# Optimization experiments

Hardware: AMD Instinct MI355X
Metric: run time of the kernel (lower is better)

## Reference

```python
import jax, jax.numpy as jnp
import numpy as np

B, G, D, H, KD, E = 64, 512, 128, 8, 16, 128
NS = 20  # num_station


def _init_w(key, shape):
    stdv = 1.0 / np.sqrt(shape[-1]).astype(np.float32)
    return jax.random.uniform(key, shape, jnp.float32, -stdv, stdv)


def setup_inputs() -> dict:
    key = jax.random.key(0)
    ks = jax.random.split(key, 12)
    return {
        "q": jax.random.normal(ks[0], (B, G, D), jnp.float32),
        "h": jax.random.normal(ks[1], (B, G, D), jnp.float32),
        "W_query_depot": _init_w(ks[2], (H, D, KD)),
        "W_key_custom": _init_w(ks[3], (H, D, KD)),
        "W_val_custom": _init_w(ks[4], (H, D, KD)),
        "W_query_station": _init_w(ks[5], (H, D, KD)),
        "W_key_other": _init_w(ks[6], (H, D, KD)),
        "W_val_other": _init_w(ks[7], (H, D, KD)),
        "W_query_custom": _init_w(ks[8], (H, D, KD)),
        "W_key_all": _init_w(ks[9], (H, D, KD)),
        "W_val_all": _init_w(ks[10], (H, D, KD)),
        "W_out": _init_w(ks[11], (H, KD, E)),
        "num_station": NS,
    }


def _mha_block(q_seg, h_seg, Wq, Wk, Wv, norm):
    # q_seg: [B, Nq, D], h_seg: [B, Nk, D]; weights: [H, D, KD]
    Q = jnp.einsum('bqd,hdk->hbqk', q_seg, Wq)
    K = jnp.einsum('bnd,hdk->hbnk', h_seg, Wk)
    V = jnp.einsum('bnd,hdk->hbnk', h_seg, Wv)
    attn = jax.nn.softmax(norm * jnp.einsum('hbqk,hbnk->hbqn', Q, K), axis=-1)
    return jnp.einsum('hbqn,hbnk->hbqk', attn, V)  # [H, B, Nq, KD]


def reference(q, h, W_query_depot, W_key_custom, W_val_custom,
              W_query_station, W_key_other, W_val_other,
              W_query_custom, W_key_all, W_val_all, W_out, num_station):
    ns = num_station
    norm = 1.0 / np.sqrt(W_query_depot.shape[-1]).astype(np.float32)
    h_custom = h[:, 1 + ns:]                                        # customers
    h_other = jnp.concatenate([h[:, :1], h[:, 1 + ns:]], axis=1)    # depot + customers
    heads_depot = _mha_block(q[:, :1], h_custom,
                             W_query_depot, W_key_custom, W_val_custom, norm)
    heads_station = _mha_block(q[:, 1:1 + ns], h_other,
                               W_query_station, W_key_other, W_val_other, norm)
    heads_custom = _mha_block(q[:, 1 + ns:], h,
                              W_query_custom, W_key_all, W_val_all, norm)
    heads = jnp.concatenate([heads_depot, heads_station, heads_custom], axis=2)
    # final projection: mm([B*G, H*KD], [H*KD, E])
    return jnp.einsum('hbgk,hke->bge', heads, W_out)
```

## Files before the change

kernel.cpp:

```cpp
#include <hip/hip_runtime.h>
#include <hip/hip_bf16.h>

namespace {

typedef _Float16 v4h __attribute__((ext_vector_type(4)));
typedef __fp16   h2  __attribute__((ext_vector_type(2)));
typedef float    v4f __attribute__((ext_vector_type(4)));

constexpr int B = 64, G = 512, D = 128, H = 8, KD = 16, NS = 20;
constexpr float NORM = 0.25f;
constexpr float L2E  = 1.44269504088896f;
constexpr float MFIX = 16.0f;
constexpr int KP = 20;
constexpr int VP = 520;
constexpr int QCH = 256;

__device__ __forceinline__ v4f mfma16(v4h a, v4h b, v4f c) {
  return __builtin_amdgcn_mfma_f32_16x16x16f16(a, b, c, 0, 0, 0);
}
__device__ __forceinline__ v4h cvt4(float4 v) {
  h2 a = __builtin_amdgcn_cvt_pkrtz(v.x, v.y);
  h2 b = __builtin_amdgcn_cvt_pkrtz(v.z, v.w);
  return v4h{(_Float16)a[0], (_Float16)a[1], (_Float16)b[0], (_Float16)b[1]};
}
__device__ __forceinline__ v4h cvtacc(v4f v) {
  h2 a = __builtin_amdgcn_cvt_pkrtz(v[0], v[1]);
  h2 b = __builtin_amdgcn_cvt_pkrtz(v[2], v[3]);
  return v4h{(_Float16)a[0], (_Float16)a[1], (_Float16)b[0], (_Float16)b[1]};
}
__device__ __forceinline__ void pexp(v4f s0, v4f s1, v4h& p0, v4h& p1) {
  h2 e01 = __builtin_amdgcn_cvt_pkrtz(__builtin_amdgcn_exp2f(s0[0]),
                                      __builtin_amdgcn_exp2f(s0[1]));
  h2 e23 = __builtin_amdgcn_cvt_pkrtz(__builtin_amdgcn_exp2f(s0[2]),
                                      __builtin_amdgcn_exp2f(s0[3]));
  h2 e45 = __builtin_amdgcn_cvt_pkrtz(__builtin_amdgcn_exp2f(s1[0]),
                                      __builtin_amdgcn_exp2f(s1[1]));
  h2 e67 = __builtin_amdgcn_cvt_pkrtz(__builtin_amdgcn_exp2f(s1[2]),
                                      __builtin_amdgcn_exp2f(s1[3]));
  p0 = {(_Float16)e01[0], (_Float16)e01[1], (_Float16)e23[0], (_Float16)e23[1]};
  p1 = {(_Float16)e45[0], (_Float16)e45[1], (_Float16)e67[0], (_Float16)e67[1]};
}

struct SM {
  char      ht[8192];
  _Float16  Kl[512 * KP];
  _Float16  Vt[16 * VP];
};

template<int SEG, bool PAIR>
__device__ __forceinline__ void attn_loop(const SM& sm, int g, int c,
                                          v4h qfA, v4h qfB,
                                          v4f& oA, v4f& laA, v4f& oB, v4f& laB)
{
  constexpr int Ln  = SEG == 0 ? G - 1 - NS : SEG == 1 ? G - NS : G;
  constexpr int NCH = (Ln + 31) / 32;
  const _Float16* Kb = sm.Kl + c * KP + 4 * g;
  const _Float16* Vb = sm.Vt + c * VP + 4 * g;
  const v4f mc = {-MFIX, -MFIX, -MFIX, -MFIX};
  const v4h ones = {(_Float16)1.f, (_Float16)1.f, (_Float16)1.f, (_Float16)1.f};

  v4h k0 = *(const v4h*)(Kb);
  v4h k1 = *(const v4h*)(Kb + 16 * KP);
  v4f s0A = mfma16(k0, qfA, mc), s1A = mfma16(k1, qfA, mc);
  v4f s0B, s1B;
  if constexpr (PAIR) { s0B = mfma16(k0, qfB, mc); s1B = mfma16(k1, qfB, mc); }

  #pragma unroll
  for (int ch = 0; ch < NCH; ++ch) {
    const int nb = ch * 32;
    const v4h v0 = *(const v4h*)(Vb + nb);
    const v4h v1 = *(const v4h*)(Vb + nb + 16);
    v4f n0A, n1A, n0B, n1B;
    if (ch + 1 < NCH) {
      k0 = *(const v4h*)(Kb + (nb + 32) * KP);
      k1 = *(const v4h*)(Kb + (nb + 48) * KP);
      n0A = mfma16(k0, qfA, mc); n1A = mfma16(k1, qfA, mc);
      if constexpr (PAIR) { n0B = mfma16(k0, qfB, mc); n1B = mfma16(k1, qfB, mc); }
    }
    if constexpr ((Ln & 31) != 0) {
      if (ch == NCH - 1) {
        #pragma unroll
        for (int r = 0; r < 4; ++r) {
          if (nb + 4 * g + r >= Ln)      { s0A[r] = -1e30f; if constexpr (PAIR) s0B[r] = -1e30f; }
          if (nb + 16 + 4 * g + r >= Ln) { s1A[r] = -1e30f; if constexpr (PAIR) s1B[r] = -1e30f; }
        }
      }
    }
    v4h p0, p1;
    pexp(s0A, s1A, p0, p1);
    oA  = mfma16(v0, p0, oA);
    oA  = mfma16(v1, p1, oA);
    laA = mfma16(ones, p0, laA);
    laA = mfma16(ones, p1, laA);
    if constexpr (PAIR) {
      pexp(s0B, s1B, p0, p1);
      oB  = mfma16(v0, p0, oB);
      oB  = mfma16(v1, p1, oB);
      laB = mfma16(ones, p0, laB);
      laB = mfma16(ones, p1, laB);
      s0B = n0B; s1B = n1B;
    }
    s0A = n0A; s1A = n1A;
  }
}

template<int SEG>
__device__ __forceinline__ void seg_body(
    int bid, const float* __restrict__ q, const float* __restrict__ hb,
    const float* __restrict__ Wq, const float* __restrict__ Wk,
    const float* __restrict__ Wv, float* __restrict__ heads, SM& sm)
{
  constexpr int Lq   = SEG == 0 ? 1 : SEG == 1 ? NS : G - 1 - NS;
  constexpr int QOFF = SEG == 0 ? 0 : SEG == 1 ? 1  : 1 + NS;
  constexpr int Ln   = SEG == 0 ? G - 1 - NS : SEG == 1 ? G - NS : G;
  constexpr int NQC  = (Lq + QCH - 1) / QCH;

  const int hh   = bid >> 6;
  const int b    = bid & 63;
  const int tid  = threadIdx.x;
  const int w    = tid >> 6;
  const int lane = tid & 63;
  const int g    = lane >> 4, c = lane & 15;

  float4 rg[2];

  {
    v4h wA[8];
    const float* Wt = (w < 4) ? Wk : Wv;
    #pragma unroll
    for (int dc = 0; dc < 8; ++dc)
      #pragma unroll
      for (int bb = 0; bb < 4; ++bb)
        wA[dc][bb] = (_Float16)Wt[((size_t)hh * D + dc * 16 + 4 * g + bb) * KD + c];

    const int wk = w & 3;
    #pragma unroll
    for (int i = 0; i < 2; ++i) {
      int idx = tid + i * 512, r = idx >> 5, jj = idx & 31;
      int nn = r < Ln ? r : Ln - 1;
      int hr;
      if (SEG == 0)      hr = nn + 1 + NS;
      else if (SEG == 1) hr = (nn == 0) ? 0 : nn + NS;
      else               hr = nn;
      rg[i] = ((const float4*)(hb + ((size_t)b * G + hr) * D))[jj];
    }
    for (int t = 0; t < 16; ++t) {
      __syncthreads();
      #pragma unroll
      for (int i = 0; i < 2; ++i) {
        int idx = tid + i * 512, r = idx >> 5, jj = idx & 31;
        *(v4h*)(sm.ht + r * 256 + ((8 * jj) ^ ((r & 7) << 4))) = cvt4(rg[i]);
      }
      if (t < 15) {
        #pragma unroll
        for (int i = 0; i < 2; ++i) {
          int idx = tid + i * 512, r = idx >> 5, jj = idx & 31;
          int n = (t + 1) * 32 + r;
          int nn = n < Ln ? n : Ln - 1;
          int hr;
          if (SEG == 0)      hr = nn + 1 + NS;
          else if (SEG == 1) hr = (nn == 0) ? 0 : nn + NS;
          else               hr = nn;
          rg[i] = ((const float4*)(hb + ((size_t)b * G + hr) * D))[jj];
        }
      }
      __syncthreads();
      const int sl = (wk - 2 * t) & 3;
      if (sl < 2) {
        const int tile = 2 * t + sl;
        v4f acc = {0.f, 0.f, 0.f, 0.f};
        #pragma unroll
        for (int dc = 0; dc < 8; ++dc) {
          const v4h a = *(const v4h*)(sm.ht + (sl * 16 + c) * 256 +
                                      ((32 * dc + 8 * g) ^ ((c & 7) << 4)));
          acc = mfma16(a, wA[dc], acc);
        }
        if (w < 4) {
          #pragma unroll
          for (int r = 0; r < 4; ++r)
            sm.Kl[(tile * 16 + 4 * g + r) * KP + c] = (_Float16)acc[r];
        } else {
          v4h vv = {(_Float16)acc[0], (_Float16)acc[1], (_Float16)acc[2], (_Float16)acc[3]};
          *(v4h*)(sm.Vt + c * VP + tile * 16 + 4 * g) = vv;
        }
      }
    }
  }

  for (int qc = 0; qc < NQC; ++qc) {
    const int qbase = qc * QCH;
    const int qcnt  = (Lq - qbase < QCH) ? (Lq - qbase) : QCH;
    const int nqt   = (qcnt + 15) >> 4;
    const int nri   = (qcnt + 31) >> 5;

    v4h wQ[8];
    #pragma unroll
    for (int dc = 0; dc < 8; ++dc)
      #pragma unroll
      for (int bb = 0; bb < 4; ++bb)
        wQ[dc][bb] = (_Float16)(Wq[((size_t)hh * D + dc * 16 + 4 * g + bb) * KD + c]
                                * (NORM * L2E));

    v4f accA = {0.f,0.f,0.f,0.f}, accB = {0.f,0.f,0.f,0.f};
    #pragma unroll
    for (int i = 0; i < 2; ++i) {
      int idx = tid + i * 512, r = idx >> 5, jj = idx & 31;
      int qs = qbase + r;
      int gq = QOFF + (qs < Lq ? qs : Lq - 1);
      rg[i] = ((const float4*)(q + ((size_t)b * G + gq) * D))[jj];
    }
    for (int ri = 0; ri < nri; ++ri) {
      __syncthreads();
      #pragma unroll
      for (int i = 0; i < 2; ++i) {
        int idx = tid + i * 512, r = idx >> 5, jj = idx & 31;
        *(v4h*)(sm.ht + r * 256 + ((8 * jj) ^ ((r & 7) << 4))) = cvt4(rg[i]);
      }
      if (ri + 1 < nri) {
        #pragma unroll
        for (int i = 0; i < 2; ++i) {
          int idx = tid + i * 512, r = idx >> 5, jj = idx & 31;
          int qs = qbase + (ri + 1) * 32 + r;
          int gq = QOFF + (qs < Lq ? qs : Lq - 1);
          rg[i] = ((const float4*)(q + ((size_t)b * G + gq) * D))[jj];
        }
      }
      __syncthreads();
      const int sl = (w - 2 * ri) & 7;
      if (sl < 2) {
        const int t = 2 * ri + sl;
        if (t < nqt) {
          v4f acc = {0.f, 0.f, 0.f, 0.f};
          #pragma unroll
          for (int dc = 0; dc < 8; ++dc) {
            const v4h a = *(const v4h*)(sm.ht + (sl * 16 + c) * 256 +
                                        ((32 * dc + 8 * g) ^ ((c & 7) << 4)));
            acc = mfma16(wQ[dc], a, acc);
          }
          if (t < 8) accA = acc; else accB = acc;
        }
      }
    }

    const int t0 = w, tB = w + 8;
    const bool hasA = t0 < nqt, hasB = tB < nqt;
    if (hasA) {
      v4h qfA = cvtacc(accA);
      v4h qfB = {};
      if (hasB) qfB = cvtacc(accB);
      v4f oA = {0.f,0.f,0.f,0.f}, laA = {0.f,0.f,0.f,0.f};
      v4f oB = {0.f,0.f,0.f,0.f}, laB = {0.f,0.f,0.f,0.f};
      if (hasB) attn_loop<SEG, true >(sm, g, c, qfA, qfB, oA, laA, oB, laB);
      else      attn_loop<SEG, false>(sm, g, c, qfA, qfA, oA, laA, oB, laB);
      {
        const float invA = 1.0f / laA[0];
        const int qloc = qbase + t0 * 16 + c;
        if (qloc < Lq) {
          float4 val = {oA[0]*invA, oA[1]*invA, oA[2]*invA, oA[3]*invA};
          *(float4*)(heads + ((size_t)b * G + QOFF + qloc) * 128 + hh * 16 + 4 * g) = val;
        }
      }
      if (hasB) {
        const float invB = 1.0f / laB[0];
        const int qloc = qbase + tB * 16 + c;
        if (qloc < Lq) {
          float4 val = {oB[0]*invB, oB[1]*invB, oB[2]*invB, oB[3]*invB};
          *(float4*)(heads + ((size_t)b * G + QOFF + qloc) * 128 + hh * 16 + 4 * g) = val;
        }
      }
    }
  }
}

__global__ __launch_bounds__(512, 4)
void fused_attn(const float* __restrict__ q, const float* __restrict__ hb,
                const float* __restrict__ Wqd, const float* __restrict__ Wkc,
                const float* __restrict__ Wvc, const float* __restrict__ Wqs,
                const float* __restrict__ Wko, const float* __restrict__ Wvo,
                const float* __restrict__ Wqc, const float* __restrict__ Wka,
                const float* __restrict__ Wva, float* __restrict__ heads)
{
  __shared__ SM sm;
  const int bid = blockIdx.x;
  if (bid < 512)       seg_body<2>(bid,        q, hb, Wqc, Wka, Wva, heads, sm);
  else if (bid < 1024) seg_body<1>(bid - 512,  q, hb, Wqs, Wko, Wvo, heads, sm);
  else                 seg_body<0>(bid - 1024, q, hb, Wqd, Wkc, Wvc, heads, sm);
}

__global__ __launch_bounds__(256)
void out_proj_kernel(float* __restrict__ data, const float* __restrict__ Wout)
{
  __shared__ _Float16 WlT[128 * 132];
  __shared__ _Float16 Ah [64 * 132];
  const int tid  = threadIdx.x;
  const int lane = tid & 63, w = tid >> 6;
  const int g = lane >> 4, c = lane & 15;
  const size_t rowbase = (size_t)blockIdx.x * 64;

  #pragma unroll
  for (int i = 0; i < 16; ++i) {
    int idx = tid + i * 256;
    int k = idx >> 5, c4 = (idx & 31) * 4;
    float4 v = ((const float4*)Wout)[idx];
    WlT[(c4 + 0) * 132 + k] = (_Float16)v.x;
    WlT[(c4 + 1) * 132 + k] = (_Float16)v.y;
    WlT[(c4 + 2) * 132 + k] = (_Float16)v.z;
    WlT[(c4 + 3) * 132 + k] = (_Float16)v.w;
  }
  #pragma unroll
  for (int i = 0; i < 8; ++i) {
    int idx = tid + i * 256;
    int r = idx >> 5, c4 = (idx & 31) * 4;
    float4 v = ((const float4*)(data + rowbase * 128))[idx];
    *(v4h*)(Ah + r * 132 + c4) = cvt4(v);
  }
  __syncthreads();

  v4h af[8];
  #pragma unroll
  for (int dc = 0; dc < 8; ++dc)
    af[dc] = *(const v4h*)(Ah + (w * 16 + c) * 132 + dc * 16 + 4 * g);
  #pragma unroll
  for (int ct = 0; ct < 8; ++ct) {
    v4f acc = {0.f, 0.f, 0.f, 0.f};
    #pragma unroll
    for (int dc = 0; dc < 8; ++dc) {
      const v4h bf = *(const v4h*)(WlT + (ct * 16 + c) * 132 + dc * 16 + 4 * g);
      acc = mfma16(af[dc], bf, acc);
    }
    #pragma unroll
    for (int r = 0; r < 4; ++r)
      data[(rowbase + w * 16 + 4 * g + r) * 128 + ct * 16 + c] = acc[r];
  }
}

}

extern "C" void kernel_launch(void* const* d_in, const int* in_sizes, int n_in,
                              void* d_out, int out_size, void* d_ws, size_t ws_size,
                              hipStream_t stream) {
  const float* q    = (const float*)d_in[0];
  const float* h    = (const float*)d_in[1];
  const float* Wqd  = (const float*)d_in[2];
  const float* Wkc  = (const float*)d_in[3];
  const float* Wvc  = (const float*)d_in[4];
  const float* Wqs  = (const float*)d_in[5];
  const float* Wko  = (const float*)d_in[6];
  const float* Wvo  = (const float*)d_in[7];
  const float* Wqc  = (const float*)d_in[8];
  const float* Wka  = (const float*)d_in[9];
  const float* Wva  = (const float*)d_in[10];
  const float* Wout = (const float*)d_in[11];
  float* out = (float*)d_out;

  fused_attn<<<3 * B * H, 512, 0, stream>>>(q, h, Wqd, Wkc, Wvc,
                                            Wqs, Wko, Wvo, Wqc, Wka, Wva, out);
  out_proj_kernel<<<G * B / 64, 256, 0, stream>>>(out, Wout);
}
```

Before: 68.46 us.

## Process all query tiles per wave in one pass over K/V

Removes the query-chunk loop so each wave projects and holds up to four query tiles in registers, then streams K and V from shared memory once for all of them. This cuts repeated LDS reads of K/V and an extra round of Q-projection barriers for the large segment. It raises register pressure (four output and sum accumulators live at once) and drops the prefetch of next-chunk score MFMAs, which may reduce latency hiding or cause spills.

```diff
diff --git a/kernel.cpp b/kernel.cpp
--- a/kernel.cpp
+++ b/kernel.cpp
@@ -13,7 +13,6 @@
 constexpr float MFIX = 16.0f;
 constexpr int KP = 20;
 constexpr int VP = 520;
-constexpr int QCH = 256;
 
 __device__ __forceinline__ v4f mfma16(v4h a, v4h b, v4f c) {
   return __builtin_amdgcn_mfma_f32_16x16x16f16(a, b, c, 0, 0, 0);
@@ -47,63 +46,6 @@
   _Float16  Vt[16 * VP];
 };
 
-template<int SEG, bool PAIR>
-__device__ __forceinline__ void attn_loop(const SM& sm, int g, int c,
-                                          v4h qfA, v4h qfB,
-                                          v4f& oA, v4f& laA, v4f& oB, v4f& laB)
-{
-  constexpr int Ln  = SEG == 0 ? G - 1 - NS : SEG == 1 ? G - NS : G;
-  constexpr int NCH = (Ln + 31) / 32;
-  const _Float16* Kb = sm.Kl + c * KP + 4 * g;
-  const _Float16* Vb = sm.Vt + c * VP + 4 * g;
-  const v4f mc = {-MFIX, -MFIX, -MFIX, -MFIX};
-  const v4h ones = {(_Float16)1.f, (_Float16)1.f, (_Float16)1.f, (_Float16)1.f};
-
-  v4h k0 = *(const v4h*)(Kb);
-  v4h k1 = *(const v4h*)(Kb + 16 * KP);
-  v4f s0A = mfma16(k0, qfA, mc), s1A = mfma16(k1, qfA, mc);
-  v4f s0B, s1B;
-  if constexpr (PAIR) { s0B = mfma16(k0, qfB, mc); s1B = mfma16(k1, qfB, mc); }
-
-  #pragma unroll
-  for (int ch = 0; ch < NCH; ++ch) {
-    const int nb = ch * 32;
-    const v4h v0 = *(const v4h*)(Vb + nb);
-    const v4h v1 = *(const v4h*)(Vb + nb + 16);
-    v4f n0A, n1A, n0B, n1B;
-    if (ch + 1 < NCH) {
-      k0 = *(const v4h*)(Kb + (nb + 32) * KP);
-      k1 = *(const v4h*)(Kb + (nb + 48) * KP);
-      n0A = mfma16(k0, qfA, mc); n1A = mfma16(k1, qfA, mc);
-      if constexpr (PAIR) { n0B = mfma16(k0, qfB, mc); n1B = mfma16(k1, qfB, mc); }
-    }
-    if constexpr ((Ln & 31) != 0) {
-      if (ch == NCH - 1) {
-        #pragma unroll
-        for (int r = 0; r < 4; ++r) {
-          if (nb + 4 * g + r >= Ln)      { s0A[r] = -1e30f; if constexpr (PAIR) s0B[r] = -1e30f; }
-          if (nb + 16 + 4 * g + r >= Ln) { s1A[r] = -1e30f; if constexpr (PAIR) s1B[r] = -1e30f; }
-        }
-      }
-    }
-    v4h p0, p1;
-    pexp(s0A, s1A, p0, p1);
-    oA  = mfma16(v0, p0, oA);
-    oA  = mfma16(v1, p1, oA);
-    laA = mfma16(ones, p0, laA);
-    laA = mfma16(ones, p1, laA);
-    if constexpr (PAIR) {
-      pexp(s0B, s1B, p0, p1);
-      oB  = mfma16(v0, p0, oB);
-      oB  = mfma16(v1, p1, oB);
-      laB = mfma16(ones, p0, laB);
-      laB = mfma16(ones, p1, laB);
-      s0B = n0B; s1B = n1B;
-    }
-    s0A = n0A; s1A = n1A;
-  }
-}
-
 template<int SEG>
 __device__ __forceinline__ void seg_body(
     int bid, const float* __restrict__ q, const float* __restrict__ hb,
@@ -113,7 +55,10 @@
   constexpr int Lq   = SEG == 0 ? 1 : SEG == 1 ? NS : G - 1 - NS;
   constexpr int QOFF = SEG == 0 ? 0 : SEG == 1 ? 1  : 1 + NS;
   constexpr int Ln   = SEG == 0 ? G - 1 - NS : SEG == 1 ? G - NS : G;
-  constexpr int NQC  = (Lq + QCH - 1) / QCH;
+  constexpr int NCH  = (Ln + 31) / 32;
+  constexpr int NQT  = (Lq + 15) / 16;
+  constexpr int NRI  = (Lq + 31) / 32;
+  constexpr int NRB  = (NRI + 3) / 4;
 
   const int hh   = bid >> 6;
   const int b    = bid & 63;
@@ -187,12 +132,8 @@
     }
   }
 
-  for (int qc = 0; qc < NQC; ++qc) {
-    const int qbase = qc * QCH;
-    const int qcnt  = (Lq - qbase < QCH) ? (Lq - qbase) : QCH;
-    const int nqt   = (qcnt + 15) >> 4;
-    const int nri   = (qcnt + 31) >> 5;
-
+  v4h qf[4] = {};
+  {
     v4h wQ[8];
     #pragma unroll
     for (int dc = 0; dc < 8; ++dc)
@@ -200,71 +141,98 @@
       for (int bb = 0; bb < 4; ++bb)
         wQ[dc][bb] = (_Float16)(Wq[((size_t)hh * D + dc * 16 + 4 * g + bb) * KD + c]
                                 * (NORM * L2E));
-
-    v4f accA = {0.f,0.f,0.f,0.f}, accB = {0.f,0.f,0.f,0.f};
     #pragma unroll
     for (int i = 0; i < 2; ++i) {
       int idx = tid + i * 512, r = idx >> 5, jj = idx & 31;
-      int qs = qbase + r;
-      int gq = QOFF + (qs < Lq ? qs : Lq - 1);
-      rg[i] = ((const float4*)(q + ((size_t)b * G + gq) * D))[jj];
-    }
-    for (int ri = 0; ri < nri; ++ri) {
-      __syncthreads();
-      #pragma unroll
-      for (int i = 0; i < 2; ++i) {
-        int idx = tid + i * 512, r = idx >> 5, jj = idx & 31;
-        *(v4h*)(sm.ht + r * 256 + ((8 * jj) ^ ((r & 7) << 4))) = cvt4(rg[i]);
-      }
-      if (ri + 1 < nri) {
-        #pragma unroll
-        for (int i = 0; i < 2; ++i) {
-          int idx = tid + i * 512, r = idx >> 5, jj = idx & 31;
-          int qs = qbase + (ri + 1) * 32 + r;
-          int gq = QOFF + (qs < Lq ? qs : Lq - 1);
-          rg[i] = ((const float4*)(q + ((size_t)b * G + gq) * D))[jj];
-        }
-      }
-      __syncthreads();
-      const int sl = (w - 2 * ri) & 7;
-      if (sl < 2) {
-        const int t = 2 * ri + sl;
-        if (t < nqt) {
-          v4f acc = {0.f, 0.f, 0.f, 0.f};
+      int qs = r < Lq ? r : Lq - 1;
+      rg[i] = ((const float4*)(q + ((size_t)b * G + QOFF + qs) * D))[jj];
+    }
+    #pragma unroll
+    for (int rb = 0; rb < NRB; ++rb) {
+      #pragma unroll
+      for (int rr = 0; rr < 4; ++rr) {
+        constexpr int UNUSED = 0; (void)UNUSED;
+        const int ri = rb * 4 + rr;
+        if (ri < NRI) {
+          __syncthreads();
           #pragma unroll
-          for (int dc = 0; dc < 8; ++dc) {
-            const v4h a = *(const v4h*)(sm.ht + (sl * 16 + c) * 256 +
-                                        ((32 * dc + 8 * g) ^ ((c & 7) << 4)));
-            acc = mfma16(wQ[dc], a, acc);
+          for (int i = 0; i < 2; ++i) {
+            int idx = tid + i * 512, r = idx >> 5, jj = idx & 31;
+            *(v4h*)(sm.ht + r * 256 + ((8 * jj) ^ ((r & 7) << 4))) = cvt4(rg[i]);
           }
-          if (t < 8) accA = acc; else accB = acc;
-        }
-      }
-    }
-
-    const int t0 = w, tB = w + 8;
-    const bool hasA = t0 < nqt, hasB = tB < nqt;
-    if (hasA) {
-      v4h qfA = cvtacc(accA);
-      v4h qfB = {};
-      if (hasB) qfB = cvtacc(accB);
-      v4f oA = {0.f,0.f,0.f,0.f}, laA = {0.f,0.f,0.f,0.f};
-      v4f oB = {0.f,0.f,0.f,0.f}, laB = {0.f,0.f,0.f,0.f};
-      if (hasB) attn_loop<SEG, true >(sm, g, c, qfA, qfB, oA, laA, oB, laB);
-      else      attn_loop<SEG, false>(sm, g, c, qfA, qfA, oA, laA, oB, laB);
-      {
-        const float invA = 1.0f / laA[0];
-        const int qloc = qbase + t0 * 16 + c;
+          if (ri + 1 < NRI) {
+            #pragma unroll
+            for (int i = 0; i < 2; ++i) {
+              int idx = tid + i * 512, r = idx >> 5, jj = idx & 31;
+              int qs = (ri + 1) * 32 + r;
+              if (qs >= Lq) qs = Lq - 1;
+              rg[i] = ((const float4*)(q + ((size_t)b * G + QOFF + qs) * D))[jj];
+            }
+          }
+          __syncthreads();
+          const int sl = (w - 2 * ri) & 7;
+          if (sl < 2) {
+            const int t = 2 * ri + sl;
+            if (t < NQT) {
+              v4f acc = {0.f, 0.f, 0.f, 0.f};
+              #pragma unroll
+              for (int dc = 0; dc < 8; ++dc) {
+                const v4h a = *(const v4h*)(sm.ht + (sl * 16 + c) * 256 +
+                                            ((32 * dc + 8 * g) ^ ((c & 7) << 4)));
+                acc = mfma16(wQ[dc], a, acc);
+              }
+              qf[rb] = cvtacc(acc);
+            }
+          }
+        }
+      }
+    }
+  }
+
+  {
+    const _Float16* Kb = sm.Kl + c * KP + 4 * g;
+    const _Float16* Vb = sm.Vt + c * VP + 4 * g;
+    const v4f mc = {-MFIX, -MFIX, -MFIX, -MFIX};
+    const v4h ones = {(_Float16)1.f, (_Float16)1.f, (_Float16)1.f, (_Float16)1.f};
+    v4f o[4]  = {{0.f,0.f,0.f,0.f},{0.f,0.f,0.f,0.f},{0.f,0.f,0.f,0.f},{0.f,0.f,0.f,0.f}};
+    v4f la[4] = {{0.f,0.f,0.f,0.f},{0.f,0.f,0.f,0.f},{0.f,0.f,0.f,0.f},{0.f,0.f,0.f,0.f}};
+    #pragma unroll
+    for (int ch = 0; ch < NCH; ++ch) {
+      const int nb = ch * 32;
+      const v4h k0 = *(const v4h*)(Kb + nb * KP);
+      const v4h k1 = *(const v4h*)(Kb + (nb + 16) * KP);
+      const v4h v0 = *(const v4h*)(Vb + nb);
+      const v4h v1 = *(const v4h*)(Vb + nb + 16);
+      #pragma unroll
+      for (int j = 0; j < 4; ++j) {
+        if (w + 8 * j < NQT) {
+          v4f s0 = mfma16(k0, qf[j], mc);
+          v4f s1 = mfma16(k1, qf[j], mc);
+          if constexpr ((Ln & 31) != 0) {
+            if (ch == NCH - 1) {
+              #pragma unroll
+              for (int r = 0; r < 4; ++r) {
+                if (nb + 4 * g + r >= Ln)      s0[r] = -1e30f;
+                if (nb + 16 + 4 * g + r >= Ln) s1[r] = -1e30f;
+              }
+            }
+          }
+          v4h p0, p1;
+          pexp(s0, s1, p0, p1);
+          o[j]  = mfma16(v0, p0, o[j]);
+          o[j]  = mfma16(v1, p1, o[j]);
+          la[j] = mfma16(ones, p0, la[j]);
+          la[j] = mfma16(ones, p1, la[j]);
+        }
+      }
+    }
+    #pragma unroll
+    for (int j = 0; j < 4; ++j) {
+      if (w + 8 * j < NQT) {
+        const float inv = 1.0f / la[j][0];
+        const int qloc = (w + 8 * j) * 16 + c;
         if (qloc < Lq) {
-          float4 val = {oA[0]*invA, oA[1]*invA, oA[2]*invA, oA[3]*invA};
-          *(float4*)(heads + ((size_t)b * G + QOFF + qloc) * 128 + hh * 16 + 4 * g) = val;
-        }
-      }
-      if (hasB) {
-        const float invB = 1.0f / laB[0];
-        const int qloc = qbase + tB * 16 + c;
-        if (qloc < Lq) {
-          float4 val = {oB[0]*invB, oB[1]*invB, oB[2]*invB, oB[3]*invB};
+          float4 val = {o[j][0]*inv, o[j][1]*inv, o[j][2]*inv, o[j][3]*inv};
           *(float4*)(heads + ((size_t)b * G + QOFF + qloc) * 128 + hh * 16 + 4 * g) = val;
         }
       }
```

Measured after the change: 70.36 us. +2.8%, slower.

## Split Q/K/V projections into a separate kernel writing fp16 workspace

Applied to the files above, without the earlier changes.

Projections are moved out of the per-(segment, head, batch) attention blocks into a dedicated proj_kernel. Each block of that kernel loads a 64-row slice of h and q once and computes K/V for all three segments and all heads, plus Q, writing fp16 results to the workspace. The attention kernel then only loads precomputed K/V/Q from the workspace into LDS. This removes the repeated reading and projecting of h by every head and segment block. The cost is an extra launch and a workspace round trip through global memory.

```diff
diff --git a/kernel.cpp b/kernel.cpp
--- a/kernel.cpp
+++ b/kernel.cpp
@@ -13,7 +13,7 @@
 constexpr float MFIX = 16.0f;
 constexpr int KP = 20;
 constexpr int VP = 520;
-constexpr int QCH = 256;
+constexpr size_t TS = (size_t)B * H * 512 * 16;
 
 __device__ __forceinline__ v4f mfma16(v4h a, v4h b, v4f c) {
   return __builtin_amdgcn_mfma_f32_16x16x16f16(a, b, c, 0, 0, 0);
@@ -41,14 +41,139 @@
   p1 = {(_Float16)e45[0], (_Float16)e45[1], (_Float16)e67[0], (_Float16)e67[1]};
 }
 
-struct SM {
-  char      ht[8192];
+__global__ __launch_bounds__(512)
+void proj_kernel(const float* __restrict__ q, const float* __restrict__ hb,
+                 const float* __restrict__ Wqd, const float* __restrict__ Wkc,
+                 const float* __restrict__ Wvc, const float* __restrict__ Wqs,
+                 const float* __restrict__ Wko, const float* __restrict__ Wvo,
+                 const float* __restrict__ Wqc, const float* __restrict__ Wka,
+                 const float* __restrict__ Wva, _Float16* __restrict__ ws)
+{
+  const int rt   = blockIdx.x;
+  const int b    = blockIdx.y;
+  const int tid  = threadIdx.x;
+  const int w    = tid >> 6;
+  const int lane = tid & 63;
+  const int g    = lane >> 4, c = lane & 15;
+
+  __shared__ char ht[16384];
+
+  #pragma unroll
+  for (int i = 0; i < 4; ++i) {
+    int idx = tid + i * 512, r = idx >> 5, jj = idx & 31;
+    float4 v = ((const float4*)(hb + ((size_t)b * G + rt * 64 + r) * D))[jj];
+    *(v4h*)(ht + r * 256 + ((8 * jj) ^ ((r & 7) << 4))) = cvt4(v);
+  }
+  __syncthreads();
+
+  const float* WK[3] = {Wkc, Wko, Wka};
+  const float* WV[3] = {Wvc, Wvo, Wva};
+  for (int se = 0; se < 3; ++se) {
+    for (int ty = 0; ty < 2; ++ty) {
+      const float* W = ty ? WV[se] : WK[se];
+      v4h wf[8];
+      #pragma unroll
+      for (int dc = 0; dc < 8; ++dc)
+        #pragma unroll
+        for (int bb = 0; bb < 4; ++bb)
+          wf[dc][bb] = (_Float16)W[((size_t)w * D + dc * 16 + 4 * g + bb) * KD + c];
+      _Float16* dst = ws + TS * (1 + 2 * se + ty) + (size_t)(b * H + w) * 512 * 16;
+      #pragma unroll
+      for (int s = 0; s < 4; ++s) {
+        v4f acc = {0.f, 0.f, 0.f, 0.f};
+        #pragma unroll
+        for (int dc = 0; dc < 8; ++dc) {
+          const v4h a = *(const v4h*)(ht + (s * 16 + c) * 256 +
+                                      ((32 * dc + 8 * g) ^ ((c & 7) << 4)));
+          acc = mfma16(wf[dc], a, acc);
+        }
+        v4h out = cvtacc(acc);
+        const int hr = rt * 64 + s * 16 + c;
+        int n; bool valid;
+        if (se == 2)      { n = hr; valid = true; }
+        else if (se == 1) { valid = (hr == 0) || (hr >= 1 + NS);
+                            n = (hr == 0) ? 0 : hr - NS; }
+        else              { valid = (hr >= 1 + NS); n = hr - 1 - NS; }
+        if (valid) *(v4h*)(dst + (size_t)n * 16 + 4 * g) = out;
+      }
+    }
+  }
+
+  __syncthreads();
+  #pragma unroll
+  for (int i = 0; i < 4; ++i) {
+    int idx = tid + i * 512, r = idx >> 5, jj = idx & 31;
+    float4 v = ((const float4*)(q + ((size_t)b * G + rt * 64 + r) * D))[jj];
+    *(v4h*)(ht + r * 256 + ((8 * jj) ^ ((r & 7) << 4))) = cvt4(v);
+  }
+  __syncthreads();
+  {
+    v4h wq[8];
+    #pragma unroll
+    for (int dc = 0; dc < 8; ++dc)
+      #pragma unroll
+      for (int bb = 0; bb < 4; ++bb)
+        wq[dc][bb] = (_Float16)(Wqc[((size_t)w * D + dc * 16 + 4 * g + bb) * KD + c]
+                                * (NORM * L2E));
+    _Float16* dst = ws + (size_t)(b * H + w) * 512 * 16;
+    #pragma unroll
+    for (int s = 0; s < 4; ++s) {
+      v4f acc = {0.f, 0.f, 0.f, 0.f};
+      #pragma unroll
+      for (int dc = 0; dc < 8; ++dc) {
+        const v4h a = *(const v4h*)(ht + (s * 16 + c) * 256 +
+                                    ((32 * dc + 8 * g) ^ ((c & 7) << 4)));
+        acc = mfma16(wq[dc], a, acc);
+      }
+      v4h out = cvtacc(acc);
+      if (rt == 0 && s < 2) {
+        const int gq = s * 16 + c;
+        v4h w2[8];
+        #pragma unroll
+        for (int dc = 0; dc < 8; ++dc)
+          #pragma unroll
+          for (int bb = 0; bb < 4; ++bb)
+            w2[dc][bb] = (_Float16)(Wqs[((size_t)w * D + dc * 16 + 4 * g + bb) * KD + c]
+                                    * (NORM * L2E));
+        v4f accS = {0.f, 0.f, 0.f, 0.f};
+        #pragma unroll
+        for (int dc = 0; dc < 8; ++dc) {
+          const v4h a = *(const v4h*)(ht + (s * 16 + c) * 256 +
+                                      ((32 * dc + 8 * g) ^ ((c & 7) << 4)));
+          accS = mfma16(w2[dc], a, accS);
+        }
+        v4h outS = cvtacc(accS);
+        if (s == 0) {
+          #pragma unroll
+          for (int dc = 0; dc < 8; ++dc)
+            #pragma unroll
+            for (int bb = 0; bb < 4; ++bb)
+              w2[dc][bb] = (_Float16)(Wqd[((size_t)w * D + dc * 16 + 4 * g + bb) * KD + c]
+                                      * (NORM * L2E));
+          v4f accD = {0.f, 0.f, 0.f, 0.f};
+          #pragma unroll
+          for (int dc = 0; dc < 8; ++dc) {
+            const v4h a = *(const v4h*)(ht + (s * 16 + c) * 256 +
+                                        ((32 * dc + 8 * g) ^ ((c & 7) << 4)));
+            accD = mfma16(w2[dc], a, accD);
+          }
+          out = (gq == 0) ? cvtacc(accD) : (gq <= NS ? outS : out);
+        } else {
+          out = (gq <= NS) ? outS : out;
+        }
+      }
+      *(v4h*)(dst + (size_t)(rt * 64 + s * 16 + c) * 16 + 4 * g) = out;
+    }
+  }
+}
+
+struct SMA {
   _Float16  Kl[512 * KP];
   _Float16  Vt[16 * VP];
 };
 
 template<int SEG, bool PAIR>
-__device__ __forceinline__ void attn_loop(const SM& sm, int g, int c,
+__device__ __forceinline__ void attn_loop(const SMA& sm, int g, int c,
                                           v4h qfA, v4h qfB,
                                           v4f& oA, v4f& laA, v4f& oB, v4f& laB)
 {
@@ -105,15 +230,12 @@
 }
 
 template<int SEG>
-__device__ __forceinline__ void seg_body(
-    int bid, const float* __restrict__ q, const float* __restrict__ hb,
-    const float* __restrict__ Wq, const float* __restrict__ Wk,
-    const float* __restrict__ Wv, float* __restrict__ heads, SM& sm)
+__device__ __forceinline__ void seg_attn(int bid, const _Float16* __restrict__ ws,
+                                         float* __restrict__ heads, SMA& sm)
 {
   constexpr int Lq   = SEG == 0 ? 1 : SEG == 1 ? NS : G - 1 - NS;
   constexpr int QOFF = SEG == 0 ? 0 : SEG == 1 ? 1  : 1 + NS;
-  constexpr int Ln   = SEG == 0 ? G - 1 - NS : SEG == 1 ? G - NS : G;
-  constexpr int NQC  = (Lq + QCH - 1) / QCH;
+  constexpr int NQT  = (Lq + 15) / 16;
 
   const int hh   = bid >> 6;
   const int b    = bid & 63;
@@ -122,169 +244,68 @@
   const int lane = tid & 63;
   const int g    = lane >> 4, c = lane & 15;
 
-  float4 rg[2];
+  const size_t slice = (size_t)(b * H + hh) * 512 * 16;
+  const _Float16* Kws = ws + TS * (1 + 2 * SEG) + slice;
+  const _Float16* Vws = ws + TS * (2 + 2 * SEG) + slice;
+  const _Float16* Qws = ws + slice;
 
   {
-    v4h wA[8];
-    const float* Wt = (w < 4) ? Wk : Wv;
-    #pragma unroll
-    for (int dc = 0; dc < 8; ++dc)
-      #pragma unroll
-      for (int bb = 0; bb < 4; ++bb)
-        wA[dc][bb] = (_Float16)Wt[((size_t)hh * D + dc * 16 + 4 * g + bb) * KD + c];
-
-    const int wk = w & 3;
-    #pragma unroll
-    for (int i = 0; i < 2; ++i) {
-      int idx = tid + i * 512, r = idx >> 5, jj = idx & 31;
-      int nn = r < Ln ? r : Ln - 1;
-      int hr;
-      if (SEG == 0)      hr = nn + 1 + NS;
-      else if (SEG == 1) hr = (nn == 0) ? 0 : nn + NS;
-      else               hr = nn;
-      rg[i] = ((const float4*)(hb + ((size_t)b * G + hr) * D))[jj];
-    }
-    for (int t = 0; t < 16; ++t) {
-      __syncthreads();
-      #pragma unroll
-      for (int i = 0; i < 2; ++i) {
-        int idx = tid + i * 512, r = idx >> 5, jj = idx & 31;
-        *(v4h*)(sm.ht + r * 256 + ((8 * jj) ^ ((r & 7) << 4))) = cvt4(rg[i]);
-      }
-      if (t < 15) {
-        #pragma unroll
-        for (int i = 0; i < 2; ++i) {
-          int idx = tid + i * 512, r = idx >> 5, jj = idx & 31;
-          int n = (t + 1) * 32 + r;
-          int nn = n < Ln ? n : Ln - 1;
-          int hr;
-          if (SEG == 0)      hr = nn + 1 + NS;
-          else if (SEG == 1) hr = (nn == 0) ? 0 : nn + NS;
-          else               hr = nn;
-          rg[i] = ((const float4*)(hb + ((size_t)b * G + hr) * D))[jj];
-        }
-      }
-      __syncthreads();
-      const int sl = (wk - 2 * t) & 3;
-      if (sl < 2) {
-        const int tile = 2 * t + sl;
-        v4f acc = {0.f, 0.f, 0.f, 0.f};
-        #pragma unroll
-        for (int dc = 0; dc < 8; ++dc) {
-          const v4h a = *(const v4h*)(sm.ht + (sl * 16 + c) * 256 +
-                                      ((32 * dc + 8 * g) ^ ((c & 7) << 4)));
-          acc = mfma16(a, wA[dc], acc);
-        }
-        if (w < 4) {
-          #pragma unroll
-          for (int r = 0; r < 4; ++r)
-            sm.Kl[(tile * 16 + 4 * g + r) * KP + c] = (_Float16)acc[r];
-        } else {
-          v4h vv = {(_Float16)acc[0], (_Float16)acc[1], (_Float16)acc[2], (_Float16)acc[3]};
-          *(v4h*)(sm.Vt + c * VP + tile * 16 + 4 * g) = vv;
-        }
-      }
-    }
-  }
-
-  for (int qc = 0; qc < NQC; ++qc) {
-    const int qbase = qc * QCH;
-    const int qcnt  = (Lq - qbase < QCH) ? (Lq - qbase) : QCH;
-    const int nqt   = (qcnt + 15) >> 4;
-    const int nri   = (qcnt + 31) >> 5;
-
-    v4h wQ[8];
-    #pragma unroll
-    for (int dc = 0; dc < 8; ++dc)
-      #pragma unroll
-      for (int bb = 0; bb < 4; ++bb)
-        wQ[dc][bb] = (_Float16)(Wq[((size_t)hh * D + dc * 16 + 4 * g + bb) * KD + c]
-                                * (NORM * L2E));
-
-    v4f accA = {0.f,0.f,0.f,0.f}, accB = {0.f,0.f,0.f,0.f};
-    #pragma unroll
-    for (int i = 0; i < 2; ++i) {
-      int idx = tid + i * 512, r = idx >> 5, jj = idx & 31;
-      int qs = qbase + r;
-      int gq = QOFF + (qs < Lq ? qs : Lq - 1);
-      rg[i] = ((const float4*)(q + ((size_t)b * G + gq) * D))[jj];
-    }
-    for (int ri = 0; ri < nri; ++ri) {
-      __syncthreads();
-      #pragma unroll
-      for (int i = 0; i < 2; ++i) {
-        int idx = tid + i * 512, r = idx >> 5, jj = idx & 31;
-        *(v4h*)(sm.ht + r * 256 + ((8 * jj) ^ ((r & 7) << 4))) = cvt4(rg[i]);
-      }
-      if (ri + 1 < nri) {
-        #pragma unroll
-        for (int i = 0; i < 2; ++i) {
-          int idx = tid + i * 512, r = idx >> 5, jj = idx & 31;
-          int qs = qbase + (ri + 1) * 32 + r;
-          int gq = QOFF + (qs < Lq ? qs : Lq - 1);
-          rg[i] = ((const float4*)(q + ((size_t)b * G + gq) * D))[jj];
-        }
-      }
-      __syncthreads();
-      const int sl = (w - 2 * ri) & 7;
-      if (sl < 2) {
-        const int t = 2 * ri + sl;
-        if (t < nqt) {
-          v4f acc = {0.f, 0.f, 0.f, 0.f};
-          #pragma unroll
-          for (int dc = 0; dc < 8; ++dc) {
-            const v4h a = *(const v4h*)(sm.ht + (sl * 16 + c) * 256 +
-                                        ((32 * dc + 8 * g) ^ ((c & 7) << 4)));
-            acc = mfma16(wQ[dc], a, acc);
-          }
-          if (t < 8) accA = acc; else accB = acc;
-        }
-      }
-    }
-
-    const int t0 = w, tB = w + 8;
-    const bool hasA = t0 < nqt, hasB = tB < nqt;
-    if (hasA) {
-      v4h qfA = cvtacc(accA);
-      v4h qfB = {};
-      if (hasB) qfB = cvtacc(accB);
-      v4f oA = {0.f,0.f,0.f,0.f}, laA = {0.f,0.f,0.f,0.f};
-      v4f oB = {0.f,0.f,0.f,0.f}, laB = {0.f,0.f,0.f,0.f};
-      if (hasB) attn_loop<SEG, true >(sm, g, c, qfA, qfB, oA, laA, oB, laB);
-      else      attn_loop<SEG, false>(sm, g, c, qfA, qfA, oA, laA, oB, laB);
-      {
-        const float invA = 1.0f / laA[0];
-        const int qloc = qbase + t0 * 16 + c;
-        if (qloc < Lq) {
-          float4 val = {oA[0]*invA, oA[1]*invA, oA[2]*invA, oA[3]*invA};
-          *(float4*)(heads + ((size_t)b * G + QOFF + qloc) * 128 + hh * 16 + 4 * g) = val;
-        }
-      }
-      if (hasB) {
-        const float invB = 1.0f / laB[0];
-        const int qloc = qbase + tB * 16 + c;
-        if (qloc < Lq) {
-          float4 val = {oB[0]*invB, oB[1]*invB, oB[2]*invB, oB[3]*invB};
-          *(float4*)(heads + ((size_t)b * G + QOFF + qloc) * 128 + hh * 16 + 4 * g) = val;
-        }
+    const int n = tid;
+    float4 kA = ((const float4*)(Kws + (size_t)n * 16))[0];
+    float4 kB = ((const float4*)(Kws + (size_t)n * 16))[1];
+    v4h kk[4];
+    *(float4*)&kk[0] = kA; *(float4*)&kk[2] = kB;
+    #pragma unroll
+    for (int i = 0; i < 4; ++i)
+      *(v4h*)(sm.Kl + n * KP + 4 * i) = kk[i];
+    float4 vA = ((const float4*)(Vws + (size_t)n * 16))[0];
+    float4 vB = ((const float4*)(Vws + (size_t)n * 16))[1];
+    _Float16 vt[16];
+    *(float4*)&vt[0] = vA; *(float4*)&vt[8] = vB;
+    #pragma unroll
+    for (int k = 0; k < 16; ++k)
+      sm.Vt[k * VP + n] = vt[k];
+  }
+  __syncthreads();
+
+  #pragma unroll
+  for (int ps = 0; ps < 2; ++ps) {
+    const int t0 = w + 16 * ps, tB = w + 8 + 16 * ps;
+    if (t0 >= NQT) continue;
+    const bool hasB = tB < NQT;
+    v4h qfA = *(const v4h*)(Qws + (size_t)(QOFF + t0 * 16 + c) * 16 + 4 * g);
+    v4h qfB = hasB ? *(const v4h*)(Qws + (size_t)(QOFF + tB * 16 + c) * 16 + 4 * g) : qfA;
+    v4f oA = {0.f,0.f,0.f,0.f}, laA = {0.f,0.f,0.f,0.f};
+    v4f oB = {0.f,0.f,0.f,0.f}, laB = {0.f,0.f,0.f,0.f};
+    if (hasB) attn_loop<SEG, true >(sm, g, c, qfA, qfB, oA, laA, oB, laB);
+    else      attn_loop<SEG, false>(sm, g, c, qfA, qfA, oA, laA, oB, laB);
+    {
+      const float inv = 1.0f / laA[0];
+      const int qloc = t0 * 16 + c;
+      if (qloc < Lq) {
+        float4 val = {oA[0]*inv, oA[1]*inv, oA[2]*inv, oA[3]*inv};
+        *(float4*)(heads + ((size_t)b * G + QOFF + qloc) * 128 + hh * 16 + 4 * g) = val;
+      }
+    }
+    if (hasB) {
+      const float inv = 1.0f / laB[0];
+      const int qloc = tB * 16 + c;
+      if (qloc < Lq) {
+        float4 val = {oB[0]*inv, oB[1]*inv, oB[2]*inv, oB[3]*inv};
+        *(float4*)(heads + ((size_t)b * G + QOFF + qloc) * 128 + hh * 16 + 4 * g) = val;
       }
     }
   }
 }
 
 __global__ __launch_bounds__(512, 4)
-void fused_attn(const float* __restrict__ q, const float* __restrict__ hb,
-                const float* __restrict__ Wqd, const float* __restrict__ Wkc,
-                const float* __restrict__ Wvc, const float* __restrict__ Wqs,
-                const float* __restrict__ Wko, const float* __restrict__ Wvo,
-                const float* __restrict__ Wqc, const float* __restrict__ Wka,
-                const float* __restrict__ Wva, float* __restrict__ heads)
-{
-  __shared__ SM sm;
+void fused_attn(const _Float16* __restrict__ ws, float* __restrict__ heads)
+{
+  __shared__ SMA sm;
   const int bid = blockIdx.x;
-  if (bid < 512)       seg_body<2>(bid,        q, hb, Wqc, Wka, Wva, heads, sm);
-  else if (bid < 1024) seg_body<1>(bid - 512,  q, hb, Wqs, Wko, Wvo, heads, sm);
-  else                 seg_body<0>(bid - 1024, q, hb, Wqd, Wkc, Wvc, heads, sm);
+  if (bid < 512)       seg_attn<2>(bid,        ws, heads, sm);
+  else if (bid < 1024) seg_attn<1>(bid - 512,  ws, heads, sm);
+  else                 seg_attn<0>(bid - 1024, ws, heads, sm);
 }
 
 __global__ __launch_bounds__(256)
@@ -352,8 +373,10 @@
   const float* Wva  = (const float*)d_in[10];
   const float* Wout = (const float*)d_in[11];
   float* out = (float*)d_out;
-
-  fused_attn<<<3 * B * H, 512, 0, stream>>>(q, h, Wqd, Wkc, Wvc,
-                                            Wqs, Wko, Wvo, Wqc, Wka, Wva, out);
+  _Float16* ws = (_Float16*)d_ws;
+
+  proj_kernel<<<dim3(8, B), 512, 0, stream>>>(q, h, Wqd, Wkc, Wvc,
+                                              Wqs, Wko, Wvo, Wqc, Wka, Wva, ws);
+  fused_attn<<<3 * B * H, 512, 0, stream>>>(ws, out);
   out_proj_kernel<<<G * B / 64, 256, 0, stream>>>(out, Wout);
 }
```

After: 84.75 us. +23.8%, slower.
